# Performance work log

Hardware: AMD Instinct MI355X
Metric: run time of the kernel (lower is better)

The kernel has to match this reference:

```python
import jax, jax.numpy as jnp
import numpy as np

BRIGHTNESS_THRESHOLD = 0.4
NUM_BINS = 16


def _soft_histogram(x, mask):
    # x: [B, C, H, W], mask: [B, 1, H, W] (float 0/1)
    B, C, H, W = x.shape
    bin_centers = jnp.linspace(0.0, 1.0, NUM_BINS, dtype=x.dtype)  # [nb]
    bin_width = 1.0 / NUM_BINS
    inv_two_sigma2 = 1.0 / (2.0 * bin_width * bin_width)
    x_flat = x.reshape(B, C, H * W, 1)            # [B,C,HW,1]
    mask_flat = mask.reshape(B, 1, H * W, 1)      # [B,1,HW,1]
    weights = jnp.exp(-((x_flat - bin_centers) ** 2) * inv_two_sigma2)  # [B,C,HW,nb]
    hist = jnp.sum(weights * mask_flat, axis=2)   # [B,C,nb]
    hist = hist / (jnp.sum(hist, axis=-1, keepdims=True) + 1e-7)
    return hist


def setup_inputs() -> dict:
    key = jax.random.key(0)
    k1, k2 = jax.random.split(key)
    pred = jax.random.uniform(k1, (8, 3, 512, 512), dtype=jnp.float32)
    target = jax.random.uniform(k2, (8, 3, 512, 512), dtype=jnp.float32)
    return {"pred": pred, "target": target}


def reference(pred, target):
    target_brightness = jnp.mean(target, axis=1, keepdims=True)       # [B,1,H,W]
    bright_mask = (target_brightness > BRIGHTNESS_THRESHOLD).astype(pred.dtype)
    pred_hist = _soft_histogram(pred, bright_mask)
    target_hist = _soft_histogram(target, bright_mask)
    return jnp.mean(jnp.abs(pred_hist - target_hist))
```

## Files before the change

kernel.cpp:

```cpp
#include <hip/hip_runtime.h>

#define NB 16
#define BATCH 8
#define PLANE (512*512)
#define FBINS 512
#define CHUNKS 128
#define CTHREADS 512
#define PX_PER_BLOCK (PLANE / CHUNKS)
#define SLICES 8
#define FPB (FBINS / SLICES)

#if __has_builtin(__builtin_amdgcn_exp2f)
__device__ __forceinline__ float exp2_fast(float x) { return __builtin_amdgcn_exp2f(x); }
#else
__device__ __forceinline__ float exp2_fast(float x) { return __expf(x * 0.69314718056f); }
#endif

#define NEG_C2 (-0.8207331788f)

__device__ __forceinline__ int qbin(float x) {
    int f = (int)(x * (float)FBINS);
    return f > (FBINS - 1) ? (FBINS - 1) : f;
}

__global__ __launch_bounds__(CTHREADS, 8)
void count_kernel(const float* __restrict__ pred,
                  const float* __restrict__ tgt,
                  unsigned int* __restrict__ partial
                  )
{
    const int chunk = blockIdx.x;
    const int b     = blockIdx.y;
    const int tid   = threadIdx.x;

    __shared__ unsigned int cnt[3 * FBINS];
    #pragma unroll
    for (int k = 0; k < 3 * FBINS / CTHREADS; ++k)
        cnt[tid + k * CTHREADS] = 0u;
    __syncthreads();

    const float* pb = pred + (size_t)b * 3 * PLANE;
    const float* tb = tgt  + (size_t)b * 3 * PLANE;
    const int p = chunk * PX_PER_BLOCK + tid * 4;

    const float4 P0 = *(const float4*)(pb + p);
    const float4 P1 = *(const float4*)(pb + PLANE + p);
    const float4 P2 = *(const float4*)(pb + 2 * PLANE + p);
    const float4 T0 = *(const float4*)(tb + p);
    const float4 T1 = *(const float4*)(tb + PLANE + p);
    const float4 T2 = *(const float4*)(tb + 2 * PLANE + p);

    const float p0a[4] = {P0.x, P0.y, P0.z, P0.w};
    const float p1a[4] = {P1.x, P1.y, P1.z, P1.w};
    const float p2a[4] = {P2.x, P2.y, P2.z, P2.w};
    const float t0a[4] = {T0.x, T0.y, T0.z, T0.w};
    const float t1a[4] = {T1.x, T1.y, T1.z, T1.w};
    const float t2a[4] = {T2.x, T2.y, T2.z, T2.w};

    #pragma unroll
    for (int j = 0; j < 4; ++j) {
        const bool m = (t0a[j] + t1a[j] + t2a[j]) * (1.0f / 3.0f) > 0.4f;
        if (m) {
            atomicAdd(&cnt[           qbin(p0a[j])], 1u);
            atomicAdd(&cnt[           qbin(p1a[j])], 65536u);
            atomicAdd(&cnt[FBINS    + qbin(p2a[j])], 1u);
            atomicAdd(&cnt[FBINS    + qbin(t0a[j])], 65536u);
            atomicAdd(&cnt[2*FBINS  + qbin(t1a[j])], 1u);
            atomicAdd(&cnt[2*FBINS  + qbin(t2a[j])], 65536u);
        }
    }
    __syncthreads();

    #pragma unroll
    for (int k = 0; k < 3 * FBINS / CTHREADS; ++k) {
        const int w  = tid + k * CTHREADS;
        const int h2 = w >> 9;
        const int f  = w & (FBINS - 1);
        partial[(((size_t)h2 * BATCH + b) * CHUNKS + chunk) * FBINS + f] = cnt[w];
    }
}

__global__ __launch_bounds__(256)
void combine_kernel(const unsigned int* __restrict__ partial,
                    float* __restrict__ out2 )
{
    const int slice = blockIdx.x;
    const int hb    = blockIdx.y;
    const int h     = hb / BATCH;
    const int b     = hb % BATCH;
    const int h2    = h >> 1;
    const int sh    = (h & 1) * 16;
    const int tid   = threadIdx.x;

    const int f_loc = tid & (FPB - 1);
    const int q     = tid >> 6;
    const int f     = slice * FPB + f_loc;

    const unsigned int* base =
        partial + (((size_t)h2 * BATCH + b) * CHUNKS + q * 32) * FBINS + f;
    unsigned int s = 0u;
    #pragma unroll 8
    for (int c = 0; c < 32; ++c)
        s += (base[(size_t)c * FBINS] >> sh) & 0xFFFFu;

    __shared__ unsigned int red[4][FPB];
    red[q][f_loc] = s;
    __syncthreads();

    if (tid < FPB) {
        const float cf = (float)(red[0][tid] + red[1][tid] + red[2][tid] + red[3][tid]);
        const float y  = ((float)(slice * FPB + tid) + 0.5f) * (15.0f / (float)FBINS);

        float acc[NB];
        #pragma unroll
        for (int i = 0; i < NB; ++i) {
            const float u = y - (float)i;
            acc[i] = cf * exp2_fast(u * u * NEG_C2);
        }
        #pragma unroll
        for (int off = 32; off > 0; off >>= 1)
            #pragma unroll
            for (int i = 0; i < NB; ++i)
                acc[i] += __shfl_down(acc[i], off, 64);

        if (tid == 0) {
            float* o = out2 + ((size_t)slice * 48 + hb) * NB;
            #pragma unroll
            for (int i = 0; i < NB; ++i) o[i] = acc[i];
        }
    }
}

__global__ void finalize_kernel(const float* __restrict__ out2,
                                float* __restrict__ out)
{
    const int t = threadIdx.x;
    __shared__ float H[48 * NB];

    for (int e = t; e < 48 * NB; e += 384) {
        float v = 0.0f;
        #pragma unroll
        for (int s = 0; s < SLICES; ++s)
            v += out2[(size_t)s * 48 * NB + e];
        H[e] = v;
    }
    __syncthreads();

    const int b   = t / 48;
    const int rem = t % 48;
    const int c   = rem / NB;
    const int i   = rem % NB;

    const float* hp = H + ((c    ) * BATCH + b) * NB;
    const float* ht = H + ((c + 3) * BATCH + b) * NB;
    float sp = 0.0f, st = 0.0f;
    #pragma unroll
    for (int k = 0; k < NB; ++k) { sp += hp[k]; st += ht[k]; }

    float val = fabsf(hp[i] / (sp + 1e-7f) - ht[i] / (st + 1e-7f));

    #pragma unroll
    for (int off = 32; off > 0; off >>= 1)
        val += __shfl_down(val, off, 64);

    __shared__ float r[6];
    const int lane = t & 63, wv = t >> 6;
    if (lane == 0) r[wv] = val;
    __syncthreads();
    if (t == 0)
        out[0] = (r[0] + r[1] + r[2] + r[3] + r[4] + r[5]) * (1.0f / 384.0f);
}

extern "C" void kernel_launch(void* const* d_in, const int* in_sizes, int n_in,
                              void* d_out, int out_size, void* d_ws, size_t ws_size,
                              hipStream_t stream)
{
    const float* pred = (const float*)d_in[0];
    const float* tgt  = (const float*)d_in[1];

    unsigned int* partial = (unsigned int*)d_ws;
    float* out2 = (float*)((char*)d_ws + (size_t)3 * BATCH * CHUNKS * FBINS * 4);

    count_kernel<<<dim3(CHUNKS, BATCH), CTHREADS, 0, stream>>>(pred, tgt, partial);
    combine_kernel<<<dim3(SLICES, 48), 256, 0, stream>>>(partial, out2);
    finalize_kernel<<<1, 384, 0, stream>>>(out2, (float*)d_out);
}
```

Measured before the change: 88.93 us.

## Fuse finalize into combine via last-block atomic pattern and packed-pair reads

Drops the separate finalize kernel. Each combine block now atomically adds its partial histograms into a global buffer, and the last block to finish, found with an atomic counter, computes the final loss. Combine blocks also decode both 16-bit halves of each packed count word, so every partial word is read once instead of twice and the grid shrinks from 48 to 24 rows. This removes a kernel launch and halves combine's partial-buffer traffic. In exchange it relies on float atomics, which make summation order nondeterministic, and on clearing the histogram and counter inside the count kernel.

```diff
diff --git a/kernel.cpp b/kernel.cpp
--- a/kernel.cpp
+++ b/kernel.cpp
@@ -9,6 +9,8 @@
 #define PX_PER_BLOCK (PLANE / CHUNKS)
 #define SLICES 8
 #define FPB (FBINS / SLICES)
+#define NPAIR 24
+#define NHIST (48 * NB)
 
 #if __has_builtin(__builtin_amdgcn_exp2f)
 __device__ __forceinline__ float exp2_fast(float x) { return __builtin_amdgcn_exp2f(x); }
@@ -26,12 +28,18 @@
 __global__ __launch_bounds__(CTHREADS, 8)
 void count_kernel(const float* __restrict__ pred,
                   const float* __restrict__ tgt,
-                  unsigned int* __restrict__ partial
-                  )
+                  unsigned int* __restrict__ partial,
+                  float* __restrict__ hist,
+                  unsigned int* __restrict__ counter)
 {
     const int chunk = blockIdx.x;
     const int b     = blockIdx.y;
     const int tid   = threadIdx.x;
+
+    if (chunk == 0 && b == 0) {
+        for (int e = tid; e < NHIST; e += CTHREADS) hist[e] = 0.0f;
+        if (tid == 0) *counter = 0u;
+    }
 
     __shared__ unsigned int cnt[3 * FBINS];
     #pragma unroll
@@ -82,14 +90,14 @@
 
 __global__ __launch_bounds__(256)
 void combine_kernel(const unsigned int* __restrict__ partial,
-                    float* __restrict__ out2 )
+                    float* __restrict__ hist,
+                    unsigned int* __restrict__ counter,
+                    float* __restrict__ out)
 {
     const int slice = blockIdx.x;
-    const int hb    = blockIdx.y;
-    const int h     = hb / BATCH;
-    const int b     = hb % BATCH;
-    const int h2    = h >> 1;
-    const int sh    = (h & 1) * 16;
+    const int pr    = blockIdx.y;
+    const int h2    = pr / BATCH;
+    const int b     = pr % BATCH;
     const int tid   = threadIdx.x;
 
     const int f_loc = tid & (FPB - 1);
@@ -98,77 +106,89 @@
 
     const unsigned int* base =
         partial + (((size_t)h2 * BATCH + b) * CHUNKS + q * 32) * FBINS + f;
-    unsigned int s = 0u;
+    unsigned int slo = 0u, shi = 0u;
     #pragma unroll 8
-    for (int c = 0; c < 32; ++c)
-        s += (base[(size_t)c * FBINS] >> sh) & 0xFFFFu;
-
-    __shared__ unsigned int red[4][FPB];
-    red[q][f_loc] = s;
+    for (int c = 0; c < 32; ++c) {
+        const unsigned int w = base[(size_t)c * FBINS];
+        slo += w & 0xFFFFu;
+        shi += w >> 16;
+    }
+
+    __shared__ unsigned int rlo[4][FPB];
+    __shared__ unsigned int rhi[4][FPB];
+    rlo[q][f_loc] = slo;
+    rhi[q][f_loc] = shi;
     __syncthreads();
 
     if (tid < FPB) {
-        const float cf = (float)(red[0][tid] + red[1][tid] + red[2][tid] + red[3][tid]);
-        const float y  = ((float)(slice * FPB + tid) + 0.5f) * (15.0f / (float)FBINS);
-
-        float acc[NB];
+        const float clo = (float)(rlo[0][tid] + rlo[1][tid] + rlo[2][tid] + rlo[3][tid]);
+        const float chi = (float)(rhi[0][tid] + rhi[1][tid] + rhi[2][tid] + rhi[3][tid]);
+        const float y   = ((float)(slice * FPB + tid) + 0.5f) * (15.0f / (float)FBINS);
+
+        float alo[NB], ahi[NB];
         #pragma unroll
         for (int i = 0; i < NB; ++i) {
             const float u = y - (float)i;
-            acc[i] = cf * exp2_fast(u * u * NEG_C2);
+            const float w = exp2_fast(u * u * NEG_C2);
+            alo[i] = clo * w;
+            ahi[i] = chi * w;
         }
         #pragma unroll
-        for (int off = 32; off > 0; off >>= 1)
+        for (int off = 32; off > 0; off >>= 1) {
             #pragma unroll
-            for (int i = 0; i < NB; ++i)
-                acc[i] += __shfl_down(acc[i], off, 64);
-
+            for (int i = 0; i < NB; ++i) {
+                alo[i] += __shfl_down(alo[i], off, 64);
+                ahi[i] += __shfl_down(ahi[i], off, 64);
+            }
+        }
         if (tid == 0) {
-            float* o = out2 + ((size_t)slice * 48 + hb) * NB;
+            const int hb_lo = (2 * h2    ) * BATCH + b;
+            const int hb_hi = (2 * h2 + 1) * BATCH + b;
             #pragma unroll
-            for (int i = 0; i < NB; ++i) o[i] = acc[i];
-        }
-    }
-}
-
-__global__ void finalize_kernel(const float* __restrict__ out2,
-                                float* __restrict__ out)
-{
-    const int t = threadIdx.x;
-    __shared__ float H[48 * NB];
-
-    for (int e = t; e < 48 * NB; e += 384) {
-        float v = 0.0f;
+            for (int i = 0; i < NB; ++i) {
+                atomicAdd(&hist[hb_lo * NB + i], alo[i]);
+                atomicAdd(&hist[hb_hi * NB + i], ahi[i]);
+            }
+        }
+    }
+
+    __threadfence();
+    __shared__ unsigned int is_last;
+    if (tid == 0)
+        is_last = (atomicAdd(counter, 1u) == SLICES * NPAIR - 1) ? 1u : 0u;
+    __syncthreads();
+    if (!is_last) return;
+
+    __threadfence();
+    __shared__ float H[NHIST];
+    for (int e = tid; e < NHIST; e += 256)
+        H[e] = atomicAdd(&hist[e], 0.0f);
+    __syncthreads();
+
+    float val = 0.0f;
+    for (int t = tid; t < 384; t += 256) {
+        const int bb  = t / 48;
+        const int rem = t % 48;
+        const int c   = rem / NB;
+        const int i   = rem % NB;
+        const float* hp = H + ((c    ) * BATCH + bb) * NB;
+        const float* ht = H + ((c + 3) * BATCH + bb) * NB;
+        float sp = 0.0f, st = 0.0f;
         #pragma unroll
-        for (int s = 0; s < SLICES; ++s)
-            v += out2[(size_t)s * 48 * NB + e];
-        H[e] = v;
-    }
-    __syncthreads();
-
-    const int b   = t / 48;
-    const int rem = t % 48;
-    const int c   = rem / NB;
-    const int i   = rem % NB;
-
-    const float* hp = H + ((c    ) * BATCH + b) * NB;
-    const float* ht = H + ((c + 3) * BATCH + b) * NB;
-    float sp = 0.0f, st = 0.0f;
-    #pragma unroll
-    for (int k = 0; k < NB; ++k) { sp += hp[k]; st += ht[k]; }
-
-    float val = fabsf(hp[i] / (sp + 1e-7f) - ht[i] / (st + 1e-7f));
+        for (int k = 0; k < NB; ++k) { sp += hp[k]; st += ht[k]; }
+        val += fabsf(hp[i] / (sp + 1e-7f) - ht[i] / (st + 1e-7f));
+    }
 
     #pragma unroll
     for (int off = 32; off > 0; off >>= 1)
         val += __shfl_down(val, off, 64);
 
-    __shared__ float r[6];
-    const int lane = t & 63, wv = t >> 6;
+    __shared__ float r[4];
+    const int lane = tid & 63, wv = tid >> 6;
     if (lane == 0) r[wv] = val;
     __syncthreads();
-    if (t == 0)
-        out[0] = (r[0] + r[1] + r[2] + r[3] + r[4] + r[5]) * (1.0f / 384.0f);
+    if (tid == 0)
+        out[0] = (r[0] + r[1] + r[2] + r[3]) * (1.0f / 384.0f);
 }
 
 extern "C" void kernel_launch(void* const* d_in, const int* in_sizes, int n_in,
@@ -178,10 +198,13 @@
     const float* pred = (const float*)d_in[0];
     const float* tgt  = (const float*)d_in[1];
 
+    const size_t part_bytes = (size_t)3 * BATCH * CHUNKS * FBINS * 4;
     unsigned int* partial = (unsigned int*)d_ws;
-    float* out2 = (float*)((char*)d_ws + (size_t)3 * BATCH * CHUNKS * FBINS * 4);
-
-    count_kernel<<<dim3(CHUNKS, BATCH), CTHREADS, 0, stream>>>(pred, tgt, partial);
-    combine_kernel<<<dim3(SLICES, 48), 256, 0, stream>>>(partial, out2);
-    finalize_kernel<<<1, 384, 0, stream>>>(out2, (float*)d_out);
-}
+    float*        hist    = (float*)((char*)d_ws + part_bytes);
+    unsigned int* counter = (unsigned int*)((char*)d_ws + part_bytes + NHIST * 4);
+
+    count_kernel<<<dim3(CHUNKS, BATCH), CTHREADS, 0, stream>>>(
+        pred, tgt, partial, hist, counter);
+    combine_kernel<<<dim3(SLICES, NPAIR), 256, 0, stream>>>(
+        partial, hist, counter, (float*)d_out);
+}
```

Result: slower. 97.89 us (+10.1%).
